# Kernel optimization log

Hardware: AMD Instinct MI355X
Metric: run time of the kernel (lower is better)

## Reference

```python
import jax, jax.numpy as jnp
import numpy as np

CODE_DIMS = [32, 32, 16]   # prod = 16384 out features
FEAT_DIM = 1024
EPS = 1e-6


def setup_inputs() -> dict:
    key = jax.random.key(0)
    kx, kw = jax.random.split(key)
    x = jax.random.normal(kx, (4, 2048, FEAT_DIM), dtype=jnp.float32)
    # per-chunk trunc-normal init like _init_weights: std = sqrt(2/(feat_dim+code_dim)), clipped at +-3 std
    parts = []
    for i, cd in enumerate(CODE_DIMS):
        std = float(np.sqrt(2.0 / (FEAT_DIM + cd)))
        parts.append(std * jax.random.truncated_normal(
            jax.random.fold_in(kw, i), -3.0, 3.0, (cd, FEAT_DIM), dtype=jnp.float32))
    weight = jnp.concatenate(parts, axis=0)  # (sum(code_dims)=80, feat_dim)
    return {"x": x, "weight": weight}


def _rms_norm(y):
    var = jnp.mean(y * y, axis=-1, keepdims=True) + EPS
    return y * jax.lax.rsqrt(var)


def reference(x, weight):
    # split weight rows into the low-rank factors
    a, b, c = jnpp_split = jnp.split(weight, np.cumsum(CODE_DIMS)[:-1].tolist(), axis=0)
    # outer product over code dims, shared feature axis z -> dynamic weight (prod(code_dims), feat_dim)
    W = jnp.einsum('az,bz,cz->abcz', a, b, c).reshape(-1, weight.shape[-1])
    y = jnp.einsum('bsi,oi->bso', x, W)  # dense projection
    return _rms_norm(y)
```

## Files before the change

kernel.cpp:

```cpp
#include <hip/hip_runtime.h>
#include <hip/hip_bf16.h>

typedef unsigned short u16;
typedef __attribute__((ext_vector_type(8))) short bf16x8;
typedef __attribute__((ext_vector_type(4))) float f32x4;
typedef __attribute__((ext_vector_type(8))) unsigned short ushort8;

#define FEAT 1024
#define NOUT 16384
#define EPS 1e-6f
#define NT 16

#define GLOBAL_AS __attribute__((address_space(1)))
#define LDS_AS __attribute__((address_space(3)))

__device__ __forceinline__ void load16_to_lds(const u16* g, u16* l) {
    __builtin_amdgcn_global_load_lds((const GLOBAL_AS void*)g, (LDS_AS void*)l, 16, 0, 0);
}

__device__ __forceinline__ u16 f32_to_bf16_bits(float f) {
    __hip_bfloat16 h = __float2bfloat16(f);
    return *reinterpret_cast<u16*>(&h);
}

__device__ __forceinline__ float bf16_bits_to_f32(u16 b) {
    unsigned u = ((unsigned)b) << 16;
    float f;
    __builtin_memcpy(&f, &u, 4);
    return f;
}

__global__ void wbuild_kernel(const float* __restrict__ w, u16* __restrict__ Wb) {
    const int t  = blockIdx.x * 256 + threadIdx.x;
    const int o  = t >> 7;
    const int k0 = (t & 127) << 3;
    const int ai = o >> 9;
    const int bi = (o >> 4) & 31;
    const int ci = o & 15;
    const float* A = w + ai * FEAT + k0;
    const float* B = w + (32 + bi) * FEAT + k0;
    const float* C = w + (64 + ci) * FEAT + k0;
    ushort8 r;
#pragma unroll
    for (int j = 0; j < 8; ++j) r[j] = f32_to_bf16_bits(A[j] * B[j] * C[j]);
    *reinterpret_cast<ushort8*>(Wb + (size_t)t * 8) = r;
}

__global__ void xcast_kernel(const float* __restrict__ x, u16* __restrict__ Xb) {
    const int t = blockIdx.x * 256 + threadIdx.x;
    const float4* xv = reinterpret_cast<const float4*>(x) + (size_t)t * 2;
    const float4 f0 = xv[0];
    const float4 f1 = xv[1];
    float vals[8] = {f0.x, f0.y, f0.z, f0.w, f1.x, f1.y, f1.z, f1.w};
    ushort8 r;
#pragma unroll
    for (int j = 0; j < 8; ++j) r[j] = f32_to_bf16_bits(vals[j]);
    *reinterpret_cast<ushort8*>(Xb + (size_t)t * 8) = r;
}


#define LDSOFF(buf, isB, kh) (((buf) << 15) + ((isB) << 14) + ((kh) << 13))

#define STAGE(isB, tt, kh, buf) do {                                          \
    const u16* g = ((isB) ? gB : gA) + (size_t)(tt) * 64 + (kh) * 32 + w * 32768; \
    u16* l = lds + LDSOFF(buf, isB, kh) + w * 1024;                           \
    load16_to_lds(g, l);                                                      \
    load16_to_lds(g + 16384, l + 512);                                        \
} while (0)

#define RD_A(dst, mi, ks, buf) dst = *reinterpret_cast<const bf16x8*>(        \
    lds + LDSOFF(buf, 0, ks) + (wm * 128 + (mi) * 16 + fr) * 32 + ((kg ^ ((fr >> 1) & 3)) << 3))
#define RD_B(dst, nj, ks, buf) dst = *reinterpret_cast<const bf16x8*>(        \
    lds + LDSOFF(buf, 1, ks) + (wn * 64 + (nj) * 16 + fr) * 32 + ((kg ^ ((fr >> 1) & 3)) << 3))

#define PHASE_SYNC() do {                                                     \
    __builtin_amdgcn_sched_barrier(0);                                        \
    __builtin_amdgcn_s_barrier();                                             \
    asm volatile("s_waitcnt lgkmcnt(0)" ::: "memory");                        \
    __builtin_amdgcn_sched_barrier(0);                                        \
} while (0)

#define MFMA_Q(mibase, WAITCODE) do {                                         \
    __builtin_amdgcn_s_setprio(1);                                            \
    _Pragma("unroll")                                                         \
    for (int mi = 0; mi < 4; ++mi) {                                          \
        acc[(mibase)+mi][0] = __builtin_amdgcn_mfma_f32_16x16x32_bf16(a[mi], b[0], acc[(mibase)+mi][0], 0, 0, 0); \
        acc[(mibase)+mi][1] = __builtin_amdgcn_mfma_f32_16x16x32_bf16(a[mi], b[1], acc[(mibase)+mi][1], 0, 0, 0); \
        acc[(mibase)+mi][2] = __builtin_amdgcn_mfma_f32_16x16x32_bf16(a[mi], b[2], acc[(mibase)+mi][2], 0, 0, 0); \
        acc[(mibase)+mi][3] = __builtin_amdgcn_mfma_f32_16x16x32_bf16(a[mi], b[3], acc[(mibase)+mi][3], 0, 0, 0); \
    }                                                                         \
    __builtin_amdgcn_s_setprio(0);                                            \
    __builtin_amdgcn_sched_barrier(0);                                        \
    WAITCODE;                                                                 \
    __builtin_amdgcn_sched_barrier(0);                                        \
    __builtin_amdgcn_s_barrier();                                             \
} while (0)

#define NOWAIT ((void)0)
#define WAIT_P2(t) do {                                                       \
    if ((t) == NT - 1) { asm volatile("s_waitcnt vmcnt(0)" ::: "memory"); }   \
    else               { asm volatile("s_waitcnt vmcnt(8)" ::: "memory"); }   \
} while (0)
#define WAIT_P4(t) do {                                                       \
    if ((t) < NT - 2)       { asm volatile("s_waitcnt vmcnt(8)" ::: "memory"); } \
    else if ((t) == NT - 2) { asm volatile("s_waitcnt vmcnt(4)" ::: "memory"); } \
} while (0)

#define TILE_BODY(t, buf, nbuf) do {                                          \
                   \
    RD_A(a[0], 0, 0, buf); RD_A(a[1], 1, 0, buf);                             \
    RD_A(a[2], 2, 0, buf); RD_A(a[3], 3, 0, buf);                             \
    RD_B(b[0], 0, 0, buf); RD_B(b[1], 1, 0, buf);                             \
    RD_B(b[2], 2, 0, buf); RD_B(b[3], 3, 0, buf);                             \
    if ((t) < NT - 1) STAGE(0, (t) + 1, 1, nbuf);                             \
    PHASE_SYNC();                                                             \
    MFMA_Q(0, NOWAIT);                                                        \
                   \
    RD_A(a[0], 4, 0, buf); RD_A(a[1], 5, 0, buf);                             \
    RD_A(a[2], 6, 0, buf); RD_A(a[3], 7, 0, buf);                             \
    if ((t) < NT - 1) STAGE(1, (t) + 1, 1, nbuf);                             \
    PHASE_SYNC();                                                             \
    MFMA_Q(4, WAIT_P2(t));                                                    \
          \
    RD_A(a[0], 0, 1, buf); RD_A(a[1], 1, 1, buf);                             \
    RD_A(a[2], 2, 1, buf); RD_A(a[3], 3, 1, buf);                             \
    RD_B(b[0], 0, 1, buf); RD_B(b[1], 1, 1, buf);                             \
    RD_B(b[2], 2, 1, buf); RD_B(b[3], 3, 1, buf);                             \
    if ((t) < NT - 2) STAGE(0, (t) + 2, 0, buf);                              \
    PHASE_SYNC();                                                             \
    MFMA_Q(0, NOWAIT);                                                        \
                    \
    RD_A(a[0], 4, 1, buf); RD_A(a[1], 5, 1, buf);                             \
    RD_A(a[2], 6, 1, buf); RD_A(a[3], 7, 1, buf);                             \
    if ((t) < NT - 2) STAGE(1, (t) + 2, 0, buf);                              \
    PHASE_SYNC();                                                             \
    MFMA_Q(4, WAIT_P4(t));                                                    \
} while (0)

__global__ __launch_bounds__(512, 2) void gemm_kernel(const u16* __restrict__ Xb,
                                                      const u16* __restrict__ Wb,
                                                      u16* __restrict__ Y,
                                                      float* __restrict__ Psum) {
    __shared__ u16 lds[65536];

    const int tid  = threadIdx.x;
    const int lane = tid & 63;
    const int w    = tid >> 6;
    const int wm   = w >> 2;
    const int wn   = w & 3;
    const int fr   = lane & 15;
    const int kg   = lane >> 4;

    const int bid = blockIdx.x;
    const int xcd = bid & 7;
    const int o   = bid >> 3;
    const int cb  = xcd * 8 + (o >> 7) * 4 + (o & 3);
    const int rb  = (o >> 2) & 31;
    const int brow = rb * 256;
    const int bcol = cb * 256;

    const int srow   = lane >> 2;
    const int kchunk = (lane & 3) ^ ((lane >> 3) & 3);
    const u16* gA = Xb + (size_t)(brow + srow) * FEAT + kchunk * 8;
    const u16* gB = Wb + (size_t)(bcol + srow) * FEAT + kchunk * 8;

    f32x4 acc[8][4] = {};
    bf16x8 a[4], b[4];

    STAGE(0, 0, 0, 0);
    STAGE(1, 0, 0, 0);
    STAGE(0, 0, 1, 0);
    STAGE(1, 0, 1, 0);
    STAGE(0, 1, 0, 1);
    STAGE(1, 1, 0, 1);
    asm volatile("s_waitcnt vmcnt(8)" ::: "memory");
    __builtin_amdgcn_s_barrier();

    for (int tt = 0; tt < NT; tt += 2) {
        TILE_BODY(tt, 0, 1);
        TILE_BODY(tt + 1, 1, 0);
    }

    float* sspart = reinterpret_cast<float*>(lds);
    const int colbase = bcol + wn * 64 + fr;
#pragma unroll
    for (int mi = 0; mi < 8; ++mi) {
#pragma unroll
        for (int r = 0; r < 4; ++r) {
            const int lrow = wm * 128 + mi * 16 + kg * 4 + r;
            u16* yrow = Y + (size_t)(brow + lrow) * 32768 + colbase;
            float s = 0.f;
#pragma unroll
            for (int nj = 0; nj < 4; ++nj) {
                const float v = acc[mi][nj][r];
                s += v * v;
                yrow[nj * 16] = f32_to_bf16_bits(v);
            }
            s += __shfl_xor(s, 1, 64);
            s += __shfl_xor(s, 2, 64);
            s += __shfl_xor(s, 4, 64);
            s += __shfl_xor(s, 8, 64);
            if (fr == 0) sspart[lrow * 4 + wn] = s;
        }
    }
    __syncthreads();
    if (tid < 256) {
        const float* sp = sspart + tid * 4;
        Psum[(size_t)(brow + tid) * 64 + cb] = sp[0] + sp[1] + sp[2] + sp[3];
    }
}

__global__ __launch_bounds__(1024) void scale_kernel(const u16* __restrict__ Y,
                                                     const float* __restrict__ Psum,
                                                     float* __restrict__ out) {
    const int row = blockIdx.x;
    const int tid = threadIdx.x;
    const ushort8* yr = reinterpret_cast<const ushort8*>(Y + (size_t)row * 32768);
    const ushort8 v0 = yr[2 * tid];
    const ushort8 v1 = yr[2 * tid + 1];

    __shared__ float scs;
    if (tid < 64) {
        float s = Psum[(size_t)row * 64 + tid];
        s += __shfl_xor(s, 1, 64);
        s += __shfl_xor(s, 2, 64);
        s += __shfl_xor(s, 4, 64);
        s += __shfl_xor(s, 8, 64);
        s += __shfl_xor(s, 16, 64);
        s += __shfl_xor(s, 32, 64);
        if (tid == 0) scs = rsqrtf(s * (1.0f / (float)NOUT) + EPS);
    }
    asm volatile("s_waitcnt vmcnt(0)" ::: "memory");
    __syncthreads();
    const float sc = scs;

    float4* orow = reinterpret_cast<float4*>(out + (size_t)row * NOUT) + tid * 4;
    float4 o0, o1, o2, o3;
    o0.x = bf16_bits_to_f32(v0[0]) * sc; o0.y = bf16_bits_to_f32(v0[1]) * sc;
    o0.z = bf16_bits_to_f32(v0[2]) * sc; o0.w = bf16_bits_to_f32(v0[3]) * sc;
    o1.x = bf16_bits_to_f32(v0[4]) * sc; o1.y = bf16_bits_to_f32(v0[5]) * sc;
    o1.z = bf16_bits_to_f32(v0[6]) * sc; o1.w = bf16_bits_to_f32(v0[7]) * sc;
    o2.x = bf16_bits_to_f32(v1[0]) * sc; o2.y = bf16_bits_to_f32(v1[1]) * sc;
    o2.z = bf16_bits_to_f32(v1[2]) * sc; o2.w = bf16_bits_to_f32(v1[3]) * sc;
    o3.x = bf16_bits_to_f32(v1[4]) * sc; o3.y = bf16_bits_to_f32(v1[5]) * sc;
    o3.z = bf16_bits_to_f32(v1[6]) * sc; o3.w = bf16_bits_to_f32(v1[7]) * sc;
    orow[0] = o0; orow[1] = o1; orow[2] = o2; orow[3] = o3;
}

extern "C" void kernel_launch(void* const* d_in, const int* in_sizes, int n_in,
                              void* d_out, int out_size, void* d_ws, size_t ws_size,
                              hipStream_t stream) {
    const float* x = (const float*)d_in[0];
    const float* w = (const float*)d_in[1];
    float* out = (float*)d_out;

    const int M = in_sizes[0] / FEAT;

    u16* Wb = (u16*)d_ws;
    u16* Xb = (u16*)((char*)d_ws + (size_t)NOUT * FEAT * 2);
    float* Psum = (float*)((char*)d_ws + (size_t)(NOUT + M) * FEAT * 2);

    u16* Y = (u16*)d_out;

    wbuild_kernel<<<(NOUT * (FEAT / 8)) / 256, 256, 0, stream>>>(w, Wb);
    xcast_kernel<<<(M * FEAT / 8) / 256, 256, 0, stream>>>(x, Xb);

    const int nblk = (M / 256) * (NOUT / 256);
    gemm_kernel<<<nblk, 512, 0, stream>>>(Xb, Wb, Y, Psum);

    scale_kernel<<<M, 1024, 0, stream>>>(Y, Psum, out);
}
```

Measured before the change: 481.2 us.

## Permute weight rows for packed epilogue stores, cut barriers, move sum-of-squares to scale kernel

The weight build now permutes output rows so each lane's four accumulator columns are contiguous. This lets the GEMM epilogue write one packed 8-byte store instead of four scattered 2-byte stores. The GEMM main loop drops two of four barriers and the lgkmcnt waits per tile, so LDS reads and MFMAs interleave under compiler scheduling, at some risk to LDS read/write hazard ordering. The partial sum-of-squares reduction and Psum buffer are removed; the scale kernel instead recomputes the row norm from the bf16 values it already loads. That norm is now taken from bf16-rounded values rather than fp32 accumulators, which slightly changes precision.

```diff
diff --git a/kernel.cpp b/kernel.cpp
--- a/kernel.cpp
+++ b/kernel.cpp
@@ -32,8 +32,9 @@
 
 __global__ void wbuild_kernel(const float* __restrict__ w, u16* __restrict__ Wb) {
     const int t  = blockIdx.x * 256 + threadIdx.x;
-    const int o  = t >> 7;
+    const int p  = t >> 7;
     const int k0 = (t & 127) << 3;
+    const int o  = (p & ~63) | ((p & 15) << 2) | ((p >> 4) & 3);
     const int ai = o >> 9;
     const int bi = (o >> 4) & 31;
     const int ci = o & 15;
@@ -73,14 +74,13 @@
 #define RD_B(dst, nj, ks, buf) dst = *reinterpret_cast<const bf16x8*>(        \
     lds + LDSOFF(buf, 1, ks) + (wn * 64 + (nj) * 16 + fr) * 32 + ((kg ^ ((fr >> 1) & 3)) << 3))
 
-#define PHASE_SYNC() do {                                                     \
+#define BAR() do {                                                            \
     __builtin_amdgcn_sched_barrier(0);                                        \
     __builtin_amdgcn_s_barrier();                                             \
-    asm volatile("s_waitcnt lgkmcnt(0)" ::: "memory");                        \
     __builtin_amdgcn_sched_barrier(0);                                        \
 } while (0)
 
-#define MFMA_Q(mibase, WAITCODE) do {                                         \
+#define MFMAQ(mibase) do {                                                    \
     __builtin_amdgcn_s_setprio(1);                                            \
     _Pragma("unroll")                                                         \
     for (int mi = 0; mi < 4; ++mi) {                                          \
@@ -90,57 +90,40 @@
         acc[(mibase)+mi][3] = __builtin_amdgcn_mfma_f32_16x16x32_bf16(a[mi], b[3], acc[(mibase)+mi][3], 0, 0, 0); \
     }                                                                         \
     __builtin_amdgcn_s_setprio(0);                                            \
-    __builtin_amdgcn_sched_barrier(0);                                        \
-    WAITCODE;                                                                 \
-    __builtin_amdgcn_sched_barrier(0);                                        \
-    __builtin_amdgcn_s_barrier();                                             \
-} while (0)
-
-#define NOWAIT ((void)0)
-#define WAIT_P2(t) do {                                                       \
+} while (0)
+
+#define WAIT_H1(t) do {                                                       \
     if ((t) == NT - 1) { asm volatile("s_waitcnt vmcnt(0)" ::: "memory"); }   \
     else               { asm volatile("s_waitcnt vmcnt(8)" ::: "memory"); }   \
 } while (0)
-#define WAIT_P4(t) do {                                                       \
+#define WAIT_H2(t) do {                                                       \
     if ((t) < NT - 2)       { asm volatile("s_waitcnt vmcnt(8)" ::: "memory"); } \
     else if ((t) == NT - 2) { asm volatile("s_waitcnt vmcnt(4)" ::: "memory"); } \
 } while (0)
 
+#define HALF(kh, buf, doStage, stT, stKh, stBuf, WAITC) do {                  \
+    RD_A(a[0], 0, kh, buf); RD_A(a[1], 1, kh, buf);                           \
+    RD_A(a[2], 2, kh, buf); RD_A(a[3], 3, kh, buf);                           \
+    RD_B(b[0], 0, kh, buf); RD_B(b[1], 1, kh, buf);                           \
+    RD_B(b[2], 2, kh, buf); RD_B(b[3], 3, kh, buf);                           \
+    if (doStage) STAGE(0, stT, stKh, stBuf);                                  \
+    MFMAQ(0);                                                                 \
+    RD_A(a[0], 4, kh, buf); RD_A(a[1], 5, kh, buf);                           \
+    RD_A(a[2], 6, kh, buf); RD_A(a[3], 7, kh, buf);                           \
+    if (doStage) STAGE(1, stT, stKh, stBuf);                                  \
+    MFMAQ(4);                                                                 \
+    WAITC;                                                                    \
+    BAR();                                                                    \
+} while (0)
+
 #define TILE_BODY(t, buf, nbuf) do {                                          \
-                   \
-    RD_A(a[0], 0, 0, buf); RD_A(a[1], 1, 0, buf);                             \
-    RD_A(a[2], 2, 0, buf); RD_A(a[3], 3, 0, buf);                             \
-    RD_B(b[0], 0, 0, buf); RD_B(b[1], 1, 0, buf);                             \
-    RD_B(b[2], 2, 0, buf); RD_B(b[3], 3, 0, buf);                             \
-    if ((t) < NT - 1) STAGE(0, (t) + 1, 1, nbuf);                             \
-    PHASE_SYNC();                                                             \
-    MFMA_Q(0, NOWAIT);                                                        \
-                   \
-    RD_A(a[0], 4, 0, buf); RD_A(a[1], 5, 0, buf);                             \
-    RD_A(a[2], 6, 0, buf); RD_A(a[3], 7, 0, buf);                             \
-    if ((t) < NT - 1) STAGE(1, (t) + 1, 1, nbuf);                             \
-    PHASE_SYNC();                                                             \
-    MFMA_Q(4, WAIT_P2(t));                                                    \
-          \
-    RD_A(a[0], 0, 1, buf); RD_A(a[1], 1, 1, buf);                             \
-    RD_A(a[2], 2, 1, buf); RD_A(a[3], 3, 1, buf);                             \
-    RD_B(b[0], 0, 1, buf); RD_B(b[1], 1, 1, buf);                             \
-    RD_B(b[2], 2, 1, buf); RD_B(b[3], 3, 1, buf);                             \
-    if ((t) < NT - 2) STAGE(0, (t) + 2, 0, buf);                              \
-    PHASE_SYNC();                                                             \
-    MFMA_Q(0, NOWAIT);                                                        \
-                    \
-    RD_A(a[0], 4, 1, buf); RD_A(a[1], 5, 1, buf);                             \
-    RD_A(a[2], 6, 1, buf); RD_A(a[3], 7, 1, buf);                             \
-    if ((t) < NT - 2) STAGE(1, (t) + 2, 0, buf);                              \
-    PHASE_SYNC();                                                             \
-    MFMA_Q(4, WAIT_P4(t));                                                    \
+    HALF(0, buf, (t) < NT - 1, (t) + 1, 1, nbuf, WAIT_H1(t));                 \
+    HALF(1, buf, (t) < NT - 2, (t) + 2, 0, buf,  WAIT_H2(t));                 \
 } while (0)
 
 __global__ __launch_bounds__(512, 2) void gemm_kernel(const u16* __restrict__ Xb,
                                                       const u16* __restrict__ Wb,
-                                                      u16* __restrict__ Y,
-                                                      float* __restrict__ Psum) {
+                                                      u16* __restrict__ Y) {
     __shared__ u16 lds[65536];
 
     const int tid  = threadIdx.x;
@@ -174,44 +157,30 @@
     STAGE(0, 1, 0, 1);
     STAGE(1, 1, 0, 1);
     asm volatile("s_waitcnt vmcnt(8)" ::: "memory");
-    __builtin_amdgcn_s_barrier();
+    BAR();
 
     for (int tt = 0; tt < NT; tt += 2) {
         TILE_BODY(tt, 0, 1);
         TILE_BODY(tt + 1, 1, 0);
     }
 
-    float* sspart = reinterpret_cast<float*>(lds);
-    const int colbase = bcol + wn * 64 + fr;
+    const int colbase = bcol + wn * 64 + fr * 4;
 #pragma unroll
     for (int mi = 0; mi < 8; ++mi) {
 #pragma unroll
         for (int r = 0; r < 4; ++r) {
-            const int lrow = wm * 128 + mi * 16 + kg * 4 + r;
-            u16* yrow = Y + (size_t)(brow + lrow) * 32768 + colbase;
-            float s = 0.f;
-#pragma unroll
-            for (int nj = 0; nj < 4; ++nj) {
-                const float v = acc[mi][nj][r];
-                s += v * v;
-                yrow[nj * 16] = f32_to_bf16_bits(v);
-            }
-            s += __shfl_xor(s, 1, 64);
-            s += __shfl_xor(s, 2, 64);
-            s += __shfl_xor(s, 4, 64);
-            s += __shfl_xor(s, 8, 64);
-            if (fr == 0) sspart[lrow * 4 + wn] = s;
+            const int row = brow + wm * 128 + mi * 16 + kg * 4 + r;
+            const unsigned lo = (unsigned)f32_to_bf16_bits(acc[mi][0][r]) |
+                                ((unsigned)f32_to_bf16_bits(acc[mi][1][r]) << 16);
+            const unsigned hi = (unsigned)f32_to_bf16_bits(acc[mi][2][r]) |
+                                ((unsigned)f32_to_bf16_bits(acc[mi][3][r]) << 16);
+            uint2 pk; pk.x = lo; pk.y = hi;
+            *reinterpret_cast<uint2*>(Y + (size_t)row * 32768 + colbase) = pk;
         }
     }
-    __syncthreads();
-    if (tid < 256) {
-        const float* sp = sspart + tid * 4;
-        Psum[(size_t)(brow + tid) * 64 + cb] = sp[0] + sp[1] + sp[2] + sp[3];
-    }
 }
 
 __global__ __launch_bounds__(1024) void scale_kernel(const u16* __restrict__ Y,
-                                                     const float* __restrict__ Psum,
                                                      float* __restrict__ out) {
     const int row = blockIdx.x;
     const int tid = threadIdx.x;
@@ -219,32 +188,36 @@
     const ushort8 v0 = yr[2 * tid];
     const ushort8 v1 = yr[2 * tid + 1];
 
-    __shared__ float scs;
-    if (tid < 64) {
-        float s = Psum[(size_t)row * 64 + tid];
-        s += __shfl_xor(s, 1, 64);
-        s += __shfl_xor(s, 2, 64);
-        s += __shfl_xor(s, 4, 64);
-        s += __shfl_xor(s, 8, 64);
-        s += __shfl_xor(s, 16, 64);
-        s += __shfl_xor(s, 32, 64);
-        if (tid == 0) scs = rsqrtf(s * (1.0f / (float)NOUT) + EPS);
-    }
-    asm volatile("s_waitcnt vmcnt(0)" ::: "memory");
+    float f[16];
+#pragma unroll
+    for (int j = 0; j < 8; ++j) {
+        f[j]     = bf16_bits_to_f32(v0[j]);
+        f[8 + j] = bf16_bits_to_f32(v1[j]);
+    }
+    float ss = 0.f;
+#pragma unroll
+    for (int j = 0; j < 16; ++j) ss += f[j] * f[j];
+
+#pragma unroll
+    for (int off = 1; off < 64; off <<= 1) ss += __shfl_xor(ss, off, 64);
+    __shared__ float wss[16];
+    if ((tid & 63) == 0) wss[tid >> 6] = ss;
     __syncthreads();
-    const float sc = scs;
+    float tot = 0.f;
+#pragma unroll
+    for (int i = 0; i < 16; ++i) tot += wss[i];
+    const float sc = rsqrtf(tot * (1.0f / (float)NOUT) + EPS);
 
     float4* orow = reinterpret_cast<float4*>(out + (size_t)row * NOUT) + tid * 4;
-    float4 o0, o1, o2, o3;
-    o0.x = bf16_bits_to_f32(v0[0]) * sc; o0.y = bf16_bits_to_f32(v0[1]) * sc;
-    o0.z = bf16_bits_to_f32(v0[2]) * sc; o0.w = bf16_bits_to_f32(v0[3]) * sc;
-    o1.x = bf16_bits_to_f32(v0[4]) * sc; o1.y = bf16_bits_to_f32(v0[5]) * sc;
-    o1.z = bf16_bits_to_f32(v0[6]) * sc; o1.w = bf16_bits_to_f32(v0[7]) * sc;
-    o2.x = bf16_bits_to_f32(v1[0]) * sc; o2.y = bf16_bits_to_f32(v1[1]) * sc;
-    o2.z = bf16_bits_to_f32(v1[2]) * sc; o2.w = bf16_bits_to_f32(v1[3]) * sc;
-    o3.x = bf16_bits_to_f32(v1[4]) * sc; o3.y = bf16_bits_to_f32(v1[5]) * sc;
-    o3.z = bf16_bits_to_f32(v1[6]) * sc; o3.w = bf16_bits_to_f32(v1[7]) * sc;
-    orow[0] = o0; orow[1] = o1; orow[2] = o2; orow[3] = o3;
+#pragma unroll
+    for (int q = 0; q < 4; ++q) {
+        float4 ov;
+        ov.x = f[q * 4 + 0] * sc;
+        ov.y = f[q * 4 + 1] * sc;
+        ov.z = f[q * 4 + 2] * sc;
+        ov.w = f[q * 4 + 3] * sc;
+        orow[q] = ov;
+    }
 }
 
 extern "C" void kernel_launch(void* const* d_in, const int* in_sizes, int n_in,
@@ -258,7 +231,6 @@
 
     u16* Wb = (u16*)d_ws;
     u16* Xb = (u16*)((char*)d_ws + (size_t)NOUT * FEAT * 2);
-    float* Psum = (float*)((char*)d_ws + (size_t)(NOUT + M) * FEAT * 2);
 
     u16* Y = (u16*)d_out;
 
@@ -266,7 +238,7 @@
     xcast_kernel<<<(M * FEAT / 8) / 256, 256, 0, stream>>>(x, Xb);
 
     const int nblk = (M / 256) * (NOUT / 256);
-    gemm_kernel<<<nblk, 512, 0, stream>>>(Xb, Wb, Y, Psum);
-
-    scale_kernel<<<M, 1024, 0, stream>>>(Y, Psum, out);
-}
+    gemm_kernel<<<nblk, 512, 0, stream>>>(Xb, Wb, Y);
+
+    scale_kernel<<<M, 1024, 0, stream>>>(Y, out);
+}
```

Result: faster. 451.7 us (median of 2 runs) (-6.1%).
